# Kernel optimization log

Measured on AMD Instinct MI355X. Metric: run time of the kernel, lower is better.

## Reference

```python
import jax, jax.numpy as jnp
import numpy as np

EPS = 1e-5

def _bn(x, gamma, beta):
    # BatchNorm1d forward (batch statistics, biased variance) over node dim
    mu = x.mean(axis=0)
    var = x.var(axis=0)
    return gamma * (x - mu) * jax.lax.rsqrt(var + EPS) + beta

def _gcn_conv(x, W, b, src, dst, n):
    # PyG GCNConv: h = x @ W; symmetric norm with self-loops; scatter-add to dst
    h = x @ W                                   # [N, out]
    ones = jnp.ones(src.shape, dtype=h.dtype)
    deg = jax.ops.segment_sum(ones, dst, num_segments=n) + 1.0  # +1 self-loop
    dinv = jax.lax.rsqrt(deg)                   # deg >= 1 always
    norm = dinv[src] * dinv[dst]                # [E]
    agg = jax.ops.segment_sum(h[src] * norm[:, None], dst, num_segments=n)
    agg = agg + h * (dinv * dinv)[:, None]      # self-loop contribution
    return agg + b

def setup_inputs() -> dict:
    key = jax.random.key(0)
    ks = jax.random.split(key, 10)
    N, E = 100000, 1600000
    Din, Dh, Dout = 256, 128, 128
    e_prev = jax.random.normal(ks[0], (N, Din), dtype=jnp.float32)
    edge_index = jax.random.randint(ks[1], (2, E), 0, N, dtype=jnp.int64)
    proj_W = jax.random.normal(ks[2], (Din, Din), dtype=jnp.float32) * 0.02
    proj_b = jnp.zeros((Din,), dtype=jnp.float32)
    W1 = jax.random.normal(ks[3], (Din, Dh), dtype=jnp.float32) * 0.05
    b1 = jnp.zeros((Dh,), dtype=jnp.float32)
    gamma1 = jnp.ones((Dh,), dtype=jnp.float32)
    beta1 = jnp.zeros((Dh,), dtype=jnp.float32)
    W2 = jax.random.normal(ks[4], (Dh, Dout), dtype=jnp.float32) * 0.05
    b2 = jnp.zeros((Dout,), dtype=jnp.float32)
    gamma2 = jnp.ones((Dout,), dtype=jnp.float32)
    beta2 = jnp.zeros((Dout,), dtype=jnp.float32)
    return {"e_prev": e_prev, "edge_index": edge_index,
            "proj_W": proj_W, "proj_b": proj_b,
            "W1": W1, "b1": b1, "gamma1": gamma1, "beta1": beta1,
            "W2": W2, "b2": b2, "gamma2": gamma2, "beta2": beta2}

def reference(e_prev, edge_index, proj_W, proj_b, W1, b1, gamma1, beta1, W2, b2, gamma2, beta2):
    n = e_prev.shape[0]
    src, dst = edge_index[0], edge_index[1]
    # input_projection (input_dim != hidden_dim branch)
    x = e_prev @ proj_W + proj_b
    x = _gcn_conv(x, W1, b1, src, dst, n)
    x = _bn(x, gamma1, beta1)
    x = jax.nn.relu(x)
    # dropout(0.2) is identity in eval mode
    x = _gcn_conv(x, W2, b2, src, dst, n)
    x = _bn(x, gamma2, beta2)
    return x
```

## Files before the change

kernel.cpp:

```cpp
#include <hip/hip_runtime.h>
#include <hip/hip_bf16.h>
#include <math.h>

#define BN_EPS 1e-5f
#define CAP 6144
#define MAXB 512

typedef __attribute__((ext_vector_type(8))) short short8;
typedef __attribute__((ext_vector_type(4))) float floatx4;

__device__ inline float4 ntload4(const float* p) {
    floatx4 v = __builtin_nontemporal_load((const floatx4*)p);
    return make_float4(v.x, v.y, v.z, v.w);
}

__global__ __launch_bounds__(128) void prep_kernel(
    const float* __restrict__ PW, const float* __restrict__ W1,
    const float* __restrict__ pb, const float* __restrict__ W2,
    __hip_bfloat16* __restrict__ Wf1, __hip_bfloat16* __restrict__ Wf2,
    float* __restrict__ bc, int* __restrict__ bcursor, int nb)
{
    int bid = blockIdx.x;
    int tid = threadIdx.x;
    if (bid < 256) {
        int k = bid, c = tid;
        float acc = 0.f;
        for (int kk = 0; kk < 256; ++kk) acc = fmaf(PW[k * 256 + kk], W1[kk * 128 + c], acc);
        int kc = k >> 5, r5 = k & 31, qq = r5 >> 3, j = r5 & 7;
        int ct = c >> 4, l16 = c & 15;
        int lane = qq * 16 + l16;
        Wf1[(((kc * 8 + ct) * 64) + lane) * 8 + j] = __float2bfloat16(acc);
    } else if (bid == 256) {
        int c = tid;
        float acc = 0.f;
        for (int k = 0; k < 256; ++k) acc = fmaf(pb[k], W1[k * 128 + c], acc);
        bc[c] = acc;
    } else if (bid < 385) {
        int t = (bid - 257) * 128 + tid;
        int j    = t & 7;
        int lane = (t >> 3) & 63;
        int ct   = (t >> 9) & 7;
        int kc   = t >> 12;
        int k = kc * 32 + ((lane >> 4) & 3) * 8 + j;
        int c = ct * 16 + (lane & 15);
        Wf2[t] = __float2bfloat16(W2[k * 128 + c]);
    } else {
        int i = (bid - 385) * 128 + tid;
        if (i < nb) bcursor[i] = i * CAP;
        if (bid == 385 && tid < 2) bcursor[nb + 8 + tid] = 0;
    }
}

__global__ __launch_bounds__(256) void bucket_kernel(
    const int* __restrict__ src, const int* __restrict__ dst,
    int* __restrict__ bcursor, unsigned* __restrict__ buck, int E, int nb)
{
    __shared__ int h[MAXB], resv[MAXB], cur[MAXB];
    for (int t = threadIdx.x; t < nb; t += 256) { h[t] = 0; cur[t] = 0; }
    __syncthreads();
    int per = (E + gridDim.x - 1) / gridDim.x;
    int e0 = blockIdx.x * per;
    int e1 = min(e0 + per, E);
    for (int e = e0 + threadIdx.x; e < e1; e += 256) {
        int d = __builtin_nontemporal_load(&dst[e]);
        atomicAdd(&h[d >> 8], 1);
    }
    __syncthreads();
    for (int t = threadIdx.x; t < nb; t += 256) {
        int c = h[t];
        if (c > 0) resv[t] = atomicAdd(&bcursor[t], c);
    }
    __syncthreads();
    for (int e = e0 + threadIdx.x; e < e1; e += 256) {
        int d = __builtin_nontemporal_load(&dst[e]);
        int s = __builtin_nontemporal_load(&src[e]);
        int b = d >> 8;
        int pos = resv[b] + atomicAdd(&cur[b], 1);
        buck[pos] = ((unsigned)(d & 255) << 17) | (unsigned)s;
    }
}

__global__ __launch_bounds__(256) void csr_kernel(
    const unsigned* __restrict__ buck, const int* __restrict__ bcursor,
    int* __restrict__ cnt, int* __restrict__ rowptr, float* __restrict__ dinv,
    int* __restrict__ ssrc, int N)
{
    __shared__ int h[256], sc[256], lcur[256], redu[256];
    int b = blockIdx.x;
    int t = threadIdx.x;
    int part = 0;
    for (int i = t; i < b; i += 256) part += bcursor[i] - i * CAP;
    redu[t] = part;
    h[t] = 0;
    __syncthreads();
    for (int off = 128; off > 0; off >>= 1) {
        if (t < off) redu[t] += redu[t + off];
        __syncthreads();
    }
    int cb = redu[0];

    int base = b * CAP;
    int nB = bcursor[b] - base;
    for (int i = t; i < nB; i += 256) {
        unsigned v = buck[base + i];
        atomicAdd(&h[v >> 17], 1);
    }
    __syncthreads();
    int myc = h[t];
    sc[t] = myc;
    __syncthreads();
    for (int off = 1; off < 256; off <<= 1) {
        int x = (t >= off) ? sc[t - off] : 0;
        __syncthreads();
        sc[t] += x;
        __syncthreads();
    }
    int ex = sc[t] - myc;
    lcur[t] = ex;
    int node = b * 256 + t;
    if (node < N) {
        cnt[node]    = myc;
        rowptr[node] = cb + ex;
        dinv[node]   = rsqrtf((float)myc + 1.0f);
    }
    __syncthreads();
    for (int i = t; i < nB; i += 256) {
        unsigned v = buck[base + i];
        int dloc = v >> 17;
        int pos = cb + atomicAdd(&lcur[dloc], 1);
        ssrc[pos] = (int)(v & 0x1FFFFu);
    }
}

__device__ inline short8 cvt8(float4 a, float4 b) {
    __hip_bfloat162 p0 = __float22bfloat162_rn(make_float2(a.x, a.y));
    __hip_bfloat162 p1 = __float22bfloat162_rn(make_float2(a.z, a.w));
    __hip_bfloat162 p2 = __float22bfloat162_rn(make_float2(b.x, b.y));
    __hip_bfloat162 p3 = __float22bfloat162_rn(make_float2(b.z, b.w));
    union { short8 s; __hip_bfloat162 h[4]; } u;
    u.h[0] = p0; u.h[1] = p1; u.h[2] = p2; u.h[3] = p3;
    return u.s;
}

template <int K, bool BN>
__global__ __launch_bounds__(256) void mfma_gemm(
    const float* __restrict__ X, const short* __restrict__ Wf,
    const float* __restrict__ bias, const float* __restrict__ dinv,
    const float* __restrict__ scale, const float* __restrict__ shift,
    __hip_bfloat16* __restrict__ Hs, int N)
{
    const int wave = threadIdx.x >> 6;
    const int lane = threadIdx.x & 63;
    const int l16  = lane & 15;
    const int q    = lane >> 4;
    const int r0   = blockIdx.x * 128 + wave * 32;

    const int ra0 = min(r0 + l16, N - 1);
    const int ra1 = min(r0 + 16 + l16, N - 1);
    const float* pA0 = X + (size_t)ra0 * K + q * 8;
    const float* pA1 = X + (size_t)ra1 * K + q * 8;
    const short8* WF = (const short8*)Wf;

    floatx4 acc[2][8];
#pragma unroll
    for (int rt = 0; rt < 2; ++rt)
#pragma unroll
        for (int ct = 0; ct < 8; ++ct) { acc[rt][ct][0] = 0.f; acc[rt][ct][1] = 0.f; acc[rt][ct][2] = 0.f; acc[rt][ct][3] = 0.f; }

#pragma unroll
    for (int kc = 0; kc < K / 32; ++kc) {
        short8 b[8];
#pragma unroll
        for (int ct = 0; ct < 8; ++ct) b[ct] = WF[(kc * 8 + ct) * 64 + lane];

        float4 x00 = ntload4(pA0 + kc * 32);
        float4 x01 = ntload4(pA0 + kc * 32 + 4);
        float4 x10 = ntload4(pA1 + kc * 32);
        float4 x11 = ntload4(pA1 + kc * 32 + 4);
        if (BN) {
            float4 sc0 = *(const float4*)(scale + kc * 32 + q * 8);
            float4 sc1 = *(const float4*)(scale + kc * 32 + q * 8 + 4);
            float4 sh0 = *(const float4*)(shift + kc * 32 + q * 8);
            float4 sh1 = *(const float4*)(shift + kc * 32 + q * 8 + 4);
            x00.x = fmaxf(fmaf(x00.x, sc0.x, sh0.x), 0.f);
            x00.y = fmaxf(fmaf(x00.y, sc0.y, sh0.y), 0.f);
            x00.z = fmaxf(fmaf(x00.z, sc0.z, sh0.z), 0.f);
            x00.w = fmaxf(fmaf(x00.w, sc0.w, sh0.w), 0.f);
            x01.x = fmaxf(fmaf(x01.x, sc1.x, sh1.x), 0.f);
            x01.y = fmaxf(fmaf(x01.y, sc1.y, sh1.y), 0.f);
            x01.z = fmaxf(fmaf(x01.z, sc1.z, sh1.z), 0.f);
            x01.w = fmaxf(fmaf(x01.w, sc1.w, sh1.w), 0.f);
            x10.x = fmaxf(fmaf(x10.x, sc0.x, sh0.x), 0.f);
            x10.y = fmaxf(fmaf(x10.y, sc0.y, sh0.y), 0.f);
            x10.z = fmaxf(fmaf(x10.z, sc0.z, sh0.z), 0.f);
            x10.w = fmaxf(fmaf(x10.w, sc0.w, sh0.w), 0.f);
            x11.x = fmaxf(fmaf(x11.x, sc1.x, sh1.x), 0.f);
            x11.y = fmaxf(fmaf(x11.y, sc1.y, sh1.y), 0.f);
            x11.z = fmaxf(fmaf(x11.z, sc1.z, sh1.z), 0.f);
            x11.w = fmaxf(fmaf(x11.w, sc1.w, sh1.w), 0.f);
        }
        short8 a0 = cvt8(x00, x01);
        short8 a1 = cvt8(x10, x11);
#pragma unroll
        for (int ct = 0; ct < 8; ++ct) {
            acc[0][ct] = __builtin_amdgcn_mfma_f32_16x16x32_bf16(a0, b[ct], acc[0][ct], 0, 0, 0);
            acc[1][ct] = __builtin_amdgcn_mfma_f32_16x16x32_bf16(a1, b[ct], acc[1][ct], 0, 0, 0);
        }
    }

    float bb[8];
#pragma unroll
    for (int ct = 0; ct < 8; ++ct) bb[ct] = bias ? bias[ct * 16 + l16] : 0.f;

#pragma unroll
    for (int rt = 0; rt < 2; ++rt) {
        int rbase = r0 + rt * 16 + q * 4;
        float dv[4];
#pragma unroll
        for (int i = 0; i < 4; ++i) dv[i] = dinv[min(rbase + i, N - 1)];
#pragma unroll
        for (int ct = 0; ct < 8; ++ct) {
#pragma unroll
            for (int i = 0; i < 4; ++i) {
                int row = rbase + i;
                if (row < N)
                    Hs[(size_t)row * 128 + ct * 16 + l16] =
                        __float2bfloat16((acc[rt][ct][i] + bb[ct]) * dv[i]);
            }
        }
    }
}

__device__ inline void accrow(uint4 u, float* a) {
    a[0] += __uint_as_float(u.x << 16);
    a[1] += __uint_as_float(u.x & 0xffff0000u);
    a[2] += __uint_as_float(u.y << 16);
    a[3] += __uint_as_float(u.y & 0xffff0000u);
    a[4] += __uint_as_float(u.z << 16);
    a[5] += __uint_as_float(u.z & 0xffff0000u);
    a[6] += __uint_as_float(u.w << 16);
    a[7] += __uint_as_float(u.w & 0xffff0000u);
}

__global__ __launch_bounds__(256) void agg_gather_kernel(
    const uint4* __restrict__ Hq, const int* __restrict__ rowptr,
    const int* __restrict__ cnt, const int* __restrict__ ssrc,
    const float* __restrict__ dinv, const float* __restrict__ bias,
    float* __restrict__ Out, int node0, int N)
{
    int node = node0 + blockIdx.x * 4 + (threadIdx.x >> 6);
    if (node >= N) return;
    int lane = threadIdx.x & 63;
    int q    = lane >> 4;
    int l16  = lane & 15;

    float a0[8] = {0,0,0,0,0,0,0,0};
    float a1[8] = {0,0,0,0,0,0,0,0};
    float a2[8] = {0,0,0,0,0,0,0,0};
    float a3[8] = {0,0,0,0,0,0,0,0};

    if (q == 0) accrow(Hq[(size_t)node * 16 + l16], a0);

    int start = rowptr[node];
    int num   = cnt[node];
    int j = 0;
    for (; j + 16 <= num; j += 16) {
        int e = start + j + q;
        int s0 = ssrc[e];
        int s1 = ssrc[e + 4];
        int s2 = ssrc[e + 8];
        int s3 = ssrc[e + 12];
        uint4 u0 = Hq[(size_t)s0 * 16 + l16];
        uint4 u1 = Hq[(size_t)s1 * 16 + l16];
        uint4 u2 = Hq[(size_t)s2 * 16 + l16];
        uint4 u3 = Hq[(size_t)s3 * 16 + l16];
        accrow(u0, a0);
        accrow(u1, a1);
        accrow(u2, a2);
        accrow(u3, a3);
    }
    for (; j + 4 <= num; j += 4) {
        int s = ssrc[start + j + q];
        accrow(Hq[(size_t)s * 16 + l16], a0);
    }
    int rem = num - j;
    if (q < rem) {
        int s = ssrc[start + j + q];
        accrow(Hq[(size_t)s * 16 + l16], a1);
    }

#pragma unroll
    for (int i = 0; i < 8; ++i) {
        float v = a0[i] + a1[i] + a2[i] + a3[i];
        v += __shfl_xor(v, 16, 64);
        v += __shfl_xor(v, 32, 64);
        a0[i] = v;
    }

    if (q == 0) {
        float di = dinv[node];
        const float4* B4 = (const float4*)bias;
        float4 bb0 = B4[l16 * 2];
        float4 bb1 = B4[l16 * 2 + 1];
        float4 o0, o1;
        o0.x = fmaf(a0[0], di, bb0.x);
        o0.y = fmaf(a0[1], di, bb0.y);
        o0.z = fmaf(a0[2], di, bb0.z);
        o0.w = fmaf(a0[3], di, bb0.w);
        o1.x = fmaf(a0[4], di, bb1.x);
        o1.y = fmaf(a0[5], di, bb1.y);
        o1.z = fmaf(a0[6], di, bb1.z);
        o1.w = fmaf(a0[7], di, bb1.w);
        float4* O4 = (float4*)(Out + (size_t)node * 128 + l16 * 8);
        O4[0] = o0;
        O4[1] = o1;
    }
}

__global__ __launch_bounds__(256) void bn_stats_kernel(
    const float* __restrict__ A, float* __restrict__ partS, float* __restrict__ partQ,
    int N, int R,
    const float* __restrict__ gamma, const float* __restrict__ beta,
    float* __restrict__ scale, float* __restrict__ shift, int* __restrict__ ctr)
{
    int col4   = threadIdx.x & 31;
    int rowoff = threadIdx.x >> 5;
    int r0 = blockIdx.x * R;
    int r1 = min(r0 + R, N);
    float4 s = make_float4(0.f, 0.f, 0.f, 0.f);
    float4 qq = make_float4(0.f, 0.f, 0.f, 0.f);
#pragma unroll 4
    for (int r = r0 + rowoff; r < r1; r += 8) {
        float4 v = *(const float4*)&A[(size_t)r * 128 + col4 * 4];
        s.x += v.x; s.y += v.y; s.z += v.z; s.w += v.w;
        qq.x = fmaf(v.x, v.x, qq.x);
        qq.y = fmaf(v.y, v.y, qq.y);
        qq.z = fmaf(v.z, v.z, qq.z);
        qq.w = fmaf(v.w, v.w, qq.w);
    }
    __shared__ float4 ls[256], lq[256];
    ls[threadIdx.x] = s;
    lq[threadIdx.x] = qq;
    __syncthreads();
    if (threadIdx.x < 32) {
        float4 ts = ls[threadIdx.x], tq = lq[threadIdx.x];
#pragma unroll
        for (int k = 1; k < 8; ++k) {
            float4 xs = ls[k * 32 + threadIdx.x];
            float4 xq = lq[k * 32 + threadIdx.x];
            ts.x += xs.x; ts.y += xs.y; ts.z += xs.z; ts.w += xs.w;
            tq.x += xq.x; tq.y += xq.y; tq.z += xq.z; tq.w += xq.w;
        }
        *(float4*)&partS[(size_t)blockIdx.x * 128 + threadIdx.x * 4] = ts;
        *(float4*)&partQ[(size_t)blockIdx.x * 128 + threadIdx.x * 4] = tq;
    }
    __syncthreads();
    __shared__ int amLast;
    if (threadIdx.x == 0) {
        __threadfence();
        amLast = (atomicAdd(ctr, 1) == (int)gridDim.x - 1);
    }
    __syncthreads();
    if (!amLast) return;
    __threadfence();
    int c = threadIdx.x & 127;
    int h = threadIdx.x >> 7;
    float fs = 0.f, fq = 0.f;
    for (int b = h * 128; b < h * 128 + 128; ++b) {
        fs += partS[(size_t)b * 128 + c];
        fq += partQ[(size_t)b * 128 + c];
    }
    __shared__ float rs_[256], rq_[256];
    rs_[threadIdx.x] = fs;
    rq_[threadIdx.x] = fq;
    __syncthreads();
    if (threadIdx.x < 128) {
        float S = rs_[threadIdx.x] + rs_[threadIdx.x + 128];
        float Q = rq_[threadIdx.x] + rq_[threadIdx.x + 128];
        float m = S / (float)N;
        float v = Q / (float)N - m * m;
        float rs = rsqrtf(v + BN_EPS);
        float sc = gamma[c] * rs;
        scale[c] = sc;
        shift[c] = fmaf(-m, sc, beta[c]);
    }
}

__global__ void bn_apply_kernel(float* __restrict__ A, const float* __restrict__ scale,
                                const float* __restrict__ shift, int N) {
    int i = blockIdx.x * blockDim.x + threadIdx.x;
    if (i >= N * 32) return;
    int c4 = i & 31;
    float4 v  = ((float4*)A)[i];
    float4 sc = ((const float4*)scale)[c4];
    float4 sh = ((const float4*)shift)[c4];
    v.x = fmaf(v.x, sc.x, sh.x);
    v.y = fmaf(v.y, sc.y, sh.y);
    v.z = fmaf(v.z, sc.z, sh.z);
    v.w = fmaf(v.w, sc.w, sh.w);
    ((float4*)A)[i] = v;
}

extern "C" void kernel_launch(void* const* d_in, const int* in_sizes, int n_in,
                              void* d_out, int out_size, void* d_ws, size_t ws_size,
                              hipStream_t stream) {
    const float* e_prev = (const float*)d_in[0];
    const int*   edges  = (const int*)d_in[1];
    const float* proj_W = (const float*)d_in[2];
    const float* proj_b = (const float*)d_in[3];
    const float* W1     = (const float*)d_in[4];
    const float* b1     = (const float*)d_in[5];
    const float* gamma1 = (const float*)d_in[6];
    const float* beta1  = (const float*)d_in[7];
    const float* W2     = (const float*)d_in[8];
    const float* b2     = (const float*)d_in[9];
    const float* gamma2 = (const float*)d_in[10];
    const float* beta2  = (const float*)d_in[11];
    float* out = (float*)d_out;

    const int N = in_sizes[0] / 256;
    const int E = in_sizes[1] / 2;
    const int* src = edges;
    const int* dst = edges + E;
    const int nb = (N + 255) >> 8;
    const int R = (N + 255) / 256;

    char* p = (char*)d_ws;
    const size_t NH = (size_t)N * 128;
    __hip_bfloat16* Hs = (__hip_bfloat16*)p;  p += NH * 2;
    unsigned* buck  = (unsigned*)p; p += (size_t)nb * CAP * 4;
    int* ssrc   = (int*)p;  p += (size_t)E * 4;
    int* cnt    = (int*)p;  p += (size_t)N * 4;
    int* rowptr = (int*)p;  p += (size_t)N * 4;
    float* dinv = (float*)p; p += (size_t)N * 4;
    int* bcursor = (int*)p; p += (size_t)(nb + 16) * 4;
    float* bc   = (float*)p; p += 128 * 4;
    float* stats = (float*)p; p += 1536 * 4;
    float* partS = (float*)p; p += 256 * 128 * 4;
    float* partQ = (float*)p; p += 256 * 128 * 4;
    __hip_bfloat16* Wf1 = (__hip_bfloat16*)p; p += 256 * 128 * 2;
    __hip_bfloat16* Wf2 = (__hip_bfloat16*)p; p += 128 * 128 * 2;
    float* scale1 = stats, *shift1 = stats + 128;
    float* scale2 = stats + 256, *shift2 = stats + 384;
    int* ctr1 = bcursor + nb + 8;
    int* ctr2 = bcursor + nb + 9;

    prep_kernel<<<389, 128, 0, stream>>>(proj_W, W1, proj_b, W2, Wf1, Wf2, bc, bcursor, nb);
    bucket_kernel<<<512, 256, 0, stream>>>(src, dst, bcursor, buck, E, nb);
    csr_kernel<<<nb, 256, 0, stream>>>(buck, bcursor, cnt, rowptr, dinv, ssrc, N);

    const int gemm_grid = (N + 127) / 128;
    const int Nh = ((N / 2) + 3) & ~3;
    const int g1 = Nh / 4;
    const int g2 = (N - Nh + 3) / 4;

    mfma_gemm<256, false><<<gemm_grid, 256, 0, stream>>>(
        e_prev, (const short*)Wf1, bc, dinv, nullptr, nullptr, Hs, N);
    agg_gather_kernel<<<g1, 256, 0, stream>>>(
        (const uint4*)Hs, rowptr, cnt, ssrc, dinv, b1, out, 0, N);
    agg_gather_kernel<<<g2, 256, 0, stream>>>(
        (const uint4*)Hs, rowptr, cnt, ssrc, dinv, b1, out, Nh, N);
    bn_stats_kernel<<<256, 256, 0, stream>>>(out, partS, partQ, N, R,
                                             gamma1, beta1, scale1, shift1, ctr1);

    mfma_gemm<128, true><<<gemm_grid, 256, 0, stream>>>(
        out, (const short*)Wf2, nullptr, dinv, scale1, shift1, Hs, N);
    agg_gather_kernel<<<g1, 256, 0, stream>>>(
        (const uint4*)Hs, rowptr, cnt, ssrc, dinv, b2, out, 0, N);
    agg_gather_kernel<<<g2, 256, 0, stream>>>(
        (const uint4*)Hs, rowptr, cnt, ssrc, dinv, b2, out, Nh, N);
    bn_stats_kernel<<<256, 256, 0, stream>>>(out, partS, partQ, N, R,
                                             gamma2, beta2, scale2, shift2, ctr2);
    bn_apply_kernel<<<(N * 32 + 255) / 256, 256, 0, stream>>>(out, scale2, shift2, N);
}
```

Baseline: 571.9 us.

## Overlap first GEMM with edge bucketing and defer dinv scaling to CSR kernel

The first GEMM no longer depends on dinv. It is fused into one launch with the edge-bucketing pass, so the compute-bound GEMM blocks and the memory/atomic-bound bucketing blocks share the GPU concurrently. The dinv row scaling of H is then applied inside the CSR kernel as an extra read-modify-write pass over the bf16 H rows. The split aggregation launches are merged into one, and the prep loops are unrolled with four accumulators. In exchange it adds a second rounding to bf16 plus extra H traffic in the CSR kernel, and the heterogeneous fused kernel may reduce occupancy for the GEMM blocks.

```diff
diff --git a/kernel.cpp b/kernel.cpp
--- a/kernel.cpp
+++ b/kernel.cpp
@@ -24,17 +24,28 @@
     int tid = threadIdx.x;
     if (bid < 256) {
         int k = bid, c = tid;
-        float acc = 0.f;
-        for (int kk = 0; kk < 256; ++kk) acc = fmaf(PW[k * 256 + kk], W1[kk * 128 + c], acc);
+        float a0 = 0.f, a1 = 0.f, a2 = 0.f, a3 = 0.f;
+        for (int kk = 0; kk < 256; kk += 4) {
+            a0 = fmaf(PW[k * 256 + kk],     W1[(kk)     * 128 + c], a0);
+            a1 = fmaf(PW[k * 256 + kk + 1], W1[(kk + 1) * 128 + c], a1);
+            a2 = fmaf(PW[k * 256 + kk + 2], W1[(kk + 2) * 128 + c], a2);
+            a3 = fmaf(PW[k * 256 + kk + 3], W1[(kk + 3) * 128 + c], a3);
+        }
+        float acc = (a0 + a1) + (a2 + a3);
         int kc = k >> 5, r5 = k & 31, qq = r5 >> 3, j = r5 & 7;
         int ct = c >> 4, l16 = c & 15;
         int lane = qq * 16 + l16;
         Wf1[(((kc * 8 + ct) * 64) + lane) * 8 + j] = __float2bfloat16(acc);
     } else if (bid == 256) {
         int c = tid;
-        float acc = 0.f;
-        for (int k = 0; k < 256; ++k) acc = fmaf(pb[k], W1[k * 128 + c], acc);
-        bc[c] = acc;
+        float a0 = 0.f, a1 = 0.f, a2 = 0.f, a3 = 0.f;
+        for (int k = 0; k < 256; k += 4) {
+            a0 = fmaf(pb[k],     W1[(k)     * 128 + c], a0);
+            a1 = fmaf(pb[k + 1], W1[(k + 1) * 128 + c], a1);
+            a2 = fmaf(pb[k + 2], W1[(k + 2) * 128 + c], a2);
+            a3 = fmaf(pb[k + 3], W1[(k + 3) * 128 + c], a3);
+        }
+        bc[c] = (a0 + a1) + (a2 + a3);
     } else if (bid < 385) {
         int t = (bid - 257) * 128 + tid;
         int j    = t & 7;
@@ -51,15 +62,16 @@
     }
 }
 
-__global__ __launch_bounds__(256) void bucket_kernel(
+__device__ void bucket_body(
     const int* __restrict__ src, const int* __restrict__ dst,
-    int* __restrict__ bcursor, unsigned* __restrict__ buck, int E, int nb)
+    int* __restrict__ bcursor, unsigned* __restrict__ buck,
+    int E, int nb, int nblocks, int bid)
 {
     __shared__ int h[MAXB], resv[MAXB], cur[MAXB];
     for (int t = threadIdx.x; t < nb; t += 256) { h[t] = 0; cur[t] = 0; }
     __syncthreads();
-    int per = (E + gridDim.x - 1) / gridDim.x;
-    int e0 = blockIdx.x * per;
+    int per = (E + nblocks - 1) / nblocks;
+    int e0 = bid * per;
     int e1 = min(e0 + per, E);
     for (int e = e0 + threadIdx.x; e < e1; e += 256) {
         int d = __builtin_nontemporal_load(&dst[e]);
@@ -83,9 +95,10 @@
 __global__ __launch_bounds__(256) void csr_kernel(
     const unsigned* __restrict__ buck, const int* __restrict__ bcursor,
     int* __restrict__ cnt, int* __restrict__ rowptr, float* __restrict__ dinv,
-    int* __restrict__ ssrc, int N)
+    int* __restrict__ ssrc, uint4* __restrict__ Hq, int N)
 {
     __shared__ int h[256], sc[256], lcur[256], redu[256];
+    __shared__ float sdv[256];
     int b = blockIdx.x;
     int t = threadIdx.x;
     int part = 0;
@@ -118,10 +131,12 @@
     int ex = sc[t] - myc;
     lcur[t] = ex;
     int node = b * 256 + t;
+    float dv = rsqrtf((float)myc + 1.0f);
+    sdv[t] = dv;
     if (node < N) {
         cnt[node]    = myc;
         rowptr[node] = cb + ex;
-        dinv[node]   = rsqrtf((float)myc + 1.0f);
+        dinv[node]   = dv;
     }
     __syncthreads();
     for (int i = t; i < nB; i += 256) {
@@ -129,6 +144,31 @@
         int dloc = v >> 17;
         int pos = cb + atomicAdd(&lcur[dloc], 1);
         ssrc[pos] = (int)(v & 0x1FFFFu);
+    }
+    int rbase = b * 256;
+    int nrow  = min(256, N - rbase);
+    int l16   = t & 15;
+    for (int i = t >> 4; i < nrow; i += 16) {
+        float d = sdv[i];
+        uint4* rp = &Hq[(size_t)(rbase + i) * 16 + l16];
+        uint4 u = *rp;
+        uint4 o;
+        {
+            __hip_bfloat162 p;
+            p = __float22bfloat162_rn(make_float2(__uint_as_float(u.x << 16) * d,
+                                                  __uint_as_float(u.x & 0xffff0000u) * d));
+            o.x = *(unsigned*)&p;
+            p = __float22bfloat162_rn(make_float2(__uint_as_float(u.y << 16) * d,
+                                                  __uint_as_float(u.y & 0xffff0000u) * d));
+            o.y = *(unsigned*)&p;
+            p = __float22bfloat162_rn(make_float2(__uint_as_float(u.z << 16) * d,
+                                                  __uint_as_float(u.z & 0xffff0000u) * d));
+            o.z = *(unsigned*)&p;
+            p = __float22bfloat162_rn(make_float2(__uint_as_float(u.w << 16) * d,
+                                                  __uint_as_float(u.w & 0xffff0000u) * d));
+            o.w = *(unsigned*)&p;
+        }
+        *rp = o;
     }
 }
 
@@ -142,8 +182,9 @@
     return u.s;
 }
 
-template <int K, bool BN>
-__global__ __launch_bounds__(256) void mfma_gemm(
+template <int K, bool BN, bool DINV>
+__device__ void gemm_body(
+    int bid,
     const float* __restrict__ X, const short* __restrict__ Wf,
     const float* __restrict__ bias, const float* __restrict__ dinv,
     const float* __restrict__ scale, const float* __restrict__ shift,
@@ -153,7 +194,7 @@
     const int lane = threadIdx.x & 63;
     const int l16  = lane & 15;
     const int q    = lane >> 4;
-    const int r0   = blockIdx.x * 128 + wave * 32;
+    const int r0   = bid * 128 + wave * 32;
 
     const int ra0 = min(r0 + l16, N - 1);
     const int ra1 = min(r0 + 16 + l16, N - 1);
@@ -217,7 +258,7 @@
         int rbase = r0 + rt * 16 + q * 4;
         float dv[4];
 #pragma unroll
-        for (int i = 0; i < 4; ++i) dv[i] = dinv[min(rbase + i, N - 1)];
+        for (int i = 0; i < 4; ++i) dv[i] = DINV ? dinv[min(rbase + i, N - 1)] : 1.f;
 #pragma unroll
         for (int ct = 0; ct < 8; ++ct) {
 #pragma unroll
@@ -225,10 +266,35 @@
                 int row = rbase + i;
                 if (row < N)
                     Hs[(size_t)row * 128 + ct * 16 + l16] =
-                        __float2bfloat16((acc[rt][ct][i] + bb[ct]) * dv[i]);
+                        __float2bfloat16(DINV ? (acc[rt][ct][i] + bb[ct]) * dv[i]
+                                              : (acc[rt][ct][i] + bb[ct]));
             }
         }
     }
+}
+
+__global__ __launch_bounds__(256) void gemm1_bucket_kernel(
+    const float* __restrict__ X, const short* __restrict__ Wf,
+    const float* __restrict__ bias,
+    __hip_bfloat16* __restrict__ Hs, int N, int gemmGrid,
+    const int* __restrict__ src, const int* __restrict__ dst,
+    int* __restrict__ bcursor, unsigned* __restrict__ buck, int E, int nb,
+    int bucketGrid)
+{
+    if ((int)blockIdx.x < gemmGrid)
+        gemm_body<256, false, false>(blockIdx.x, X, Wf, bias, nullptr, nullptr, nullptr, Hs, N);
+    else
+        bucket_body(src, dst, bcursor, buck, E, nb, bucketGrid,
+                    (int)blockIdx.x - gemmGrid);
+}
+
+__global__ __launch_bounds__(256) void mfma_gemm2_kernel(
+    const float* __restrict__ X, const short* __restrict__ Wf,
+    const float* __restrict__ dinv,
+    const float* __restrict__ scale, const float* __restrict__ shift,
+    __hip_bfloat16* __restrict__ Hs, int N)
+{
+    gemm_body<128, true, true>(blockIdx.x, X, Wf, nullptr, dinv, scale, shift, Hs, N);
 }
 
 __device__ inline void accrow(uint4 u, float* a) {
@@ -246,9 +312,9 @@
     const uint4* __restrict__ Hq, const int* __restrict__ rowptr,
     const int* __restrict__ cnt, const int* __restrict__ ssrc,
     const float* __restrict__ dinv, const float* __restrict__ bias,
-    float* __restrict__ Out, int node0, int N)
-{
-    int node = node0 + blockIdx.x * 4 + (threadIdx.x >> 6);
+    float* __restrict__ Out, int N)
+{
+    int node = blockIdx.x * 4 + (threadIdx.x >> 6);
     if (node >= N) return;
     int lane = threadIdx.x & 63;
     int q    = lane >> 4;
@@ -445,30 +511,23 @@
     int* ctr1 = bcursor + nb + 8;
     int* ctr2 = bcursor + nb + 9;
 
+    const int gemm_grid = (N + 127) / 128;
+    const int bucket_grid = 512;
+
     prep_kernel<<<389, 128, 0, stream>>>(proj_W, W1, proj_b, W2, Wf1, Wf2, bc, bcursor, nb);
-    bucket_kernel<<<512, 256, 0, stream>>>(src, dst, bcursor, buck, E, nb);
-    csr_kernel<<<nb, 256, 0, stream>>>(buck, bcursor, cnt, rowptr, dinv, ssrc, N);
-
-    const int gemm_grid = (N + 127) / 128;
-    const int Nh = ((N / 2) + 3) & ~3;
-    const int g1 = Nh / 4;
-    const int g2 = (N - Nh + 3) / 4;
-
-    mfma_gemm<256, false><<<gemm_grid, 256, 0, stream>>>(
-        e_prev, (const short*)Wf1, bc, dinv, nullptr, nullptr, Hs, N);
-    agg_gather_kernel<<<g1, 256, 0, stream>>>(
-        (const uint4*)Hs, rowptr, cnt, ssrc, dinv, b1, out, 0, N);
-    agg_gather_kernel<<<g2, 256, 0, stream>>>(
-        (const uint4*)Hs, rowptr, cnt, ssrc, dinv, b1, out, Nh, N);
+    gemm1_bucket_kernel<<<gemm_grid + bucket_grid, 256, 0, stream>>>(
+        e_prev, (const short*)Wf1, bc, Hs, N, gemm_grid,
+        src, dst, bcursor, buck, E, nb, bucket_grid);
+    csr_kernel<<<nb, 256, 0, stream>>>(buck, bcursor, cnt, rowptr, dinv, ssrc,
+                                       (uint4*)Hs, N);
+    agg_gather_kernel<<<(N + 3) / 4, 256, 0, stream>>>(
+        (const uint4*)Hs, rowptr, cnt, ssrc, dinv, b1, out, N);
     bn_stats_kernel<<<256, 256, 0, stream>>>(out, partS, partQ, N, R,
                                              gamma1, beta1, scale1, shift1, ctr1);
-
-    mfma_gemm<128, true><<<gemm_grid, 256, 0, stream>>>(
-        out, (const short*)Wf2, nullptr, dinv, scale1, shift1, Hs, N);
-    agg_gather_kernel<<<g1, 256, 0, stream>>>(
-        (const uint4*)Hs, rowptr, cnt, ssrc, dinv, b2, out, 0, N);
-    agg_gather_kernel<<<g2, 256, 0, stream>>>(
-        (const uint4*)Hs, rowptr, cnt, ssrc, dinv, b2, out, Nh, N);
+    mfma_gemm2_kernel<<<gemm_grid, 256, 0, stream>>>(
+        out, (const short*)Wf2, dinv, scale1, shift1, Hs, N);
+    agg_gather_kernel<<<(N + 3) / 4, 256, 0, stream>>>(
+        (const uint4*)Hs, rowptr, cnt, ssrc, dinv, b2, out, N);
     bn_stats_kernel<<<256, 256, 0, stream>>>(out, partS, partQ, N, R,
                                              gamma2, beta2, scale2, shift2, ctr2);
     bn_apply_kernel<<<(N * 32 + 255) / 256, 256, 0, stream>>>(out, scale2, shift2, N);
```

Measured after the change: 565.4 us. No clear change (-1.1%).
